# Kernel tuning notes

Measured on AMD Instinct MI355X. Metric: run time of the kernel, lower is better.

## Reference

```python
import jax, jax.numpy as jnp
import numpy as np

B, C, H, W_SP = 4, 64, 64, 64
CI = C // 2  # inter_channels = 32
DEPTH = 64
EPS = 1e-5


def conv2d(x, w, b, pad=0, dil=1):
    out = jax.lax.conv_general_dilated(
        x, w, window_strides=(1, 1),
        padding=[(pad, pad), (pad, pad)],
        rhs_dilation=(dil, dil),
        dimension_numbers=('NCHW', 'OIHW', 'NCHW'))
    return out + b[None, :, None, None]


def setup_inputs() -> dict:
    key = jax.random.key(0)
    ks = iter(jax.random.split(key, 32))
    nrm = lambda shp, s=0.01: jax.random.normal(next(ks), shp, jnp.float32) * s
    inp = {
        'x': jax.random.normal(next(ks), (B, C, H, W_SP), jnp.float32),
        # NonlocalBlock params (init: normal(0, 0.01), bias 0)
        'g_w': nrm((CI, C, 1, 1)), 'g_b': jnp.zeros((CI,), jnp.float32),
        'theta_w': nrm((CI, C, 1, 1)), 'theta_b': jnp.zeros((CI,), jnp.float32),
        'phi_w': nrm((CI, C, 1, 1)), 'phi_b': jnp.zeros((CI,), jnp.float32),
        'Wz_w': nrm((C, CI, 1, 1)), 'Wz_b': jnp.zeros((C,), jnp.float32),
        'bn_g': jax.random.normal(next(ks), (C,), jnp.float32),  # normal_(W[1].weight, 0) -> std 1
        'bn_b': jnp.zeros((C,), jnp.float32),
        # ASPP params (torch default kaiming init approximated by small normals)
        'a_mean_w': nrm((DEPTH, C, 1, 1), 0.05), 'a_mean_b': jnp.zeros((DEPTH,), jnp.float32),
        'a1_w': nrm((DEPTH, C, 1, 1), 0.05), 'a1_b': jnp.zeros((DEPTH,), jnp.float32),
        'a3_w': nrm((DEPTH, C, 3, 3), 0.02), 'a3_b': jnp.zeros((DEPTH,), jnp.float32),
        'a5_w': nrm((DEPTH, C, 3, 3), 0.02), 'a5_b': jnp.zeros((DEPTH,), jnp.float32),
        'a7_w': nrm((DEPTH, C, 3, 3), 0.02), 'a7_b': jnp.zeros((DEPTH,), jnp.float32),
        'out_w': nrm((DEPTH, DEPTH * 5, 1, 1), 0.02), 'out_b': jnp.zeros((DEPTH,), jnp.float32),
    }
    return inp


def _forward(x, g_w, g_b, theta_w, theta_b, phi_w, phi_b, Wz_w, Wz_b, bn_g, bn_b,
             a_mean_w, a_mean_b, a1_w, a1_b, a3_w, a3_b, a5_w, a5_b, a7_w, a7_b,
             out_w, out_b):
    b, c, h, w = x.shape
    n = h * w
    # ---- NonlocalBlock: global self-attention ----
    g_x = conv2d(x, g_w, g_b).reshape(b, CI, n).transpose(0, 2, 1)       # [B,N,Ci]
    theta_x = conv2d(x, theta_w, theta_b).reshape(b, CI, n).transpose(0, 2, 1)  # [B,N,Ci]
    phi_x = conv2d(x, phi_w, phi_b).reshape(b, CI, n)                    # [B,Ci,N]
    f = jnp.einsum('bqc,bck->bqk', theta_x, phi_x)                       # [B,N,N]
    f_div_C = jax.nn.softmax(f, axis=2)
    y = jnp.einsum('bqk,bkc->bqc', f_div_C, g_x)                         # [B,N,Ci]
    y = y.transpose(0, 2, 1).reshape(b, CI, h, w)
    wy = conv2d(y, Wz_w, Wz_b)
    # BatchNorm (eval: running_mean=0, running_var=1)
    wy = wy * (bn_g / jnp.sqrt(1.0 + EPS))[None, :, None, None] + bn_b[None, :, None, None]
    z = wy + x
    # ---- ASPP ----
    img = jnp.mean(z, axis=(2, 3), keepdims=True)                        # [B,C,1,1]
    img = conv2d(img, a_mean_w, a_mean_b)                                # [B,D,1,1]
    img = jnp.broadcast_to(img, (b, DEPTH, h, w))  # bilinear upsample of 1x1 is constant
    b1 = conv2d(z, a1_w, a1_b)
    b3 = conv2d(z, a3_w, a3_b, pad=3, dil=3)
    b5 = conv2d(z, a5_w, a5_b, pad=5, dil=5)
    b7 = conv2d(z, a7_w, a7_b, pad=7, dil=7)
    cat = jnp.concatenate([img, b1, b3, b5, b7], axis=1)                 # [B,5D,H,W]
    return conv2d(cat, out_w, out_b)                                     # [B,D,H,W]


def reference(x, g_w, g_b, theta_w, theta_b, phi_w, phi_b, Wz_w, Wz_b, bn_g, bn_b,
              a_mean_w, a_mean_b, a1_w, a1_b, a3_w, a3_b, a5_w, a5_b, a7_w, a7_b,
              out_w, out_b):
    return _forward(x, g_w, g_b, theta_w, theta_b, phi_w, phi_b, Wz_w, Wz_b, bn_g, bn_b,
                    a_mean_w, a_mean_b, a1_w, a1_b, a3_w, a3_b, a5_w, a5_b, a7_w, a7_b,
                    out_w, out_b)
```

## Files before the change

### kernel.cpp

```cpp
#include <hip/hip_runtime.h>


typedef __attribute__((ext_vector_type(8))) short bf16x8;
typedef __attribute__((ext_vector_type(4))) short s16x4;
typedef __attribute__((ext_vector_type(4))) float f32x4;

#define MFMA(a, b, c) __builtin_amdgcn_mfma_f32_16x16x32_bf16((a), (b), (c), 0, 0, 0)

#if __has_builtin(__builtin_amdgcn_exp2f)
#define EXP2(x) __builtin_amdgcn_exp2f(x)
#else
#define EXP2(x) exp2f(x)
#endif

__device__ static inline short f2bf(float f) {
  union { float f; unsigned u; } v; v.f = f;
  unsigned r = v.u + 0x7fffu + ((v.u >> 16) & 1u);
  return (short)(r >> 16);
}
__device__ static inline float bf2f(unsigned short h) {
  union { unsigned u; float f; } v; v.u = ((unsigned)h) << 16;
  return v.f;
}
__device__ static inline s16x4 pk4(f32x4 v) {
  s16x4 r; r.x = f2bf(v.x); r.y = f2bf(v.y); r.z = f2bf(v.z); r.w = f2bf(v.w);
  return r;
}
__device__ static inline unsigned pk2(float f0, float f1) {
  union { float f; unsigned u; } a, b; a.f = f0; b.f = f1;
  return __builtin_amdgcn_perm(b.u, a.u, 0x07060302u);
}
__device__ static inline float unlo(unsigned d) {
  union { unsigned u; float f; } v; v.u = d << 16; return v.f;
}
__device__ static inline float unhi(unsigned d) {
  union { unsigned u; float f; } v; v.u = d & 0xffff0000u; return v.f;
}
__device__ static inline f32x4 exp24(f32x4 v) {
  f32x4 r; r.x = EXP2(v.x); r.y = EXP2(v.y); r.z = EXP2(v.z); r.w = EXP2(v.w);
  return r;
}

#define QF_PER_B 131072
#define ZPB      389376
#define LOG2E    1.4426950408889634f

__global__ __launch_bounds__(256) void k_zero(unsigned* zp, float* zmean) {
  int blk = blockIdx.x, t = threadIdx.x;
  if (blk == 996) { if (t < 256) zmean[t] = 0.f; return; }
  int b = blk / 249, loc = blk - b * 249;
  int i = loc * 256 + t;
  if (i >= 63616) return;
  int px = i >> 5, dw = i & 31;
  int row, col;
  if (px < 1092) {
    int r = px / 78; col = px - r * 78;
    row = (r < 7) ? r : r + 64;
  } else {
    int j = px - 1092;
    int r = j / 14; int c = j - r * 14;
    row = r + 7; col = (c < 7) ? c : c + 57;
  }
  zp[b * (ZPB / 2) + (row * 78 + col) * 32 + dw] = 0u;
}

__global__ __launch_bounds__(256) void k_prep(
    const float* __restrict__ out_w, const float* __restrict__ a1_w,
    const float* __restrict__ a3_w, const float* __restrict__ a5_w,
    const float* __restrict__ a7_w, const float* __restrict__ Wz_w,
    const float* __restrict__ bn_g, const float* __restrict__ Wz_b,
    const float* __restrict__ bn_b,
    unsigned short* __restrict__ Wfrag, unsigned short* __restrict__ WzF,
    float* __restrict__ bias2) {
  int blk = blockIdx.x, t = threadIdx.x;
  if (blk < 28) {
    __shared__ float wsm[4096];
    __shared__ float osm[64 * 65];
    int tap = blk;
    const float* w; int goff, kyx = 0, ksq = 9;
    if (tap == 0)      { w = a1_w; goff = 64;  ksq = 1; }
    else if (tap < 10) { w = a3_w; goff = 128; kyx = tap - 1; }
    else if (tap < 19) { w = a5_w; goff = 192; kyx = tap - 10; }
    else               { w = a7_w; goff = 256; kyx = tap - 19; }
    for (int i = t; i < 4096; i += 256) {
      wsm[i] = w[i * ksq + kyx];
      int d = i >> 6, m = i & 63;
      osm[d * 65 + m] = out_w[d * 320 + goff + m];
    }
    __syncthreads();
    int dt = t >> 6, lane = t & 63, quad = lane >> 4, l15 = lane & 15;
    int d = dt * 16 + l15;
    float acc[16];
    #pragma unroll
    for (int k = 0; k < 16; ++k) acc[k] = 0.f;
    const float* orow = osm + d * 65;
    int c0 = quad * 8;
    for (int m = 0; m < 64; ++m) {
      float o = orow[m];
      const float* wr = wsm + m * 64 + c0;
      #pragma unroll
      for (int cc = 0; cc < 2; ++cc)
        #pragma unroll
        for (int j = 0; j < 8; ++j)
          acc[cc * 8 + j] += o * wr[cc * 32 + j];
    }
    #pragma unroll
    for (int cc = 0; cc < 2; ++cc) {
      bf16x8 v;
      #pragma unroll
      for (int j = 0; j < 8; ++j) v[j] = f2bf(acc[cc * 8 + j]);
      *(bf16x8*)(Wfrag + (((tap * 4 + dt) * 2 + cc) * 64 + lane) * 8) = v;
    }
  } else if (blk == 28) {
    int ct = t >> 6, lane = t & 63, quad = lane >> 4, l15 = lane & 15;
    int c = ct * 16 + l15;
    float s = bn_g[c] * rsqrtf(1.f + 1e-5f);
    bf16x8 v;
    #pragma unroll
    for (int j = 0; j < 8; ++j) v[j] = f2bf(s * Wz_w[c * 32 + quad * 8 + j]);
    *(bf16x8*)(WzF + (ct * 64 + lane) * 8) = v;
  } else if (t < 64) {
    float s = bn_g[t] * rsqrtf(1.f + 1e-5f);
    bias2[t] = s * Wz_b[t] + bn_b[t];
  }
}

__global__ __launch_bounds__(256) void k_qkv(
    const float* __restrict__ x,
    const float* __restrict__ tw, const float* __restrict__ tb,
    const float* __restrict__ pw, const float* __restrict__ pb,
    const float* __restrict__ gw, const float* __restrict__ gb,
    unsigned short* __restrict__ thetaB, unsigned short* __restrict__ phiB,
    unsigned short* __restrict__ gB) {
  __shared__ float wl[2048];
  __shared__ float bl[32];
  int blk = blockIdx.x;
  int b = blk & 3, pt = (blk >> 2) & 15, proj = blk >> 6;
  const float* w    = proj == 0 ? tw : (proj == 1 ? pw : gw);
  const float* bias = proj == 0 ? tb : (proj == 1 ? pb : gb);
  int tid = threadIdx.x;
  for (int i = tid; i < 2048; i += 256) wl[i] = w[i];
  if (tid < 32) bl[tid] = bias[tid];
  __syncthreads();
  int pix = pt*256 + tid;
  const float* xp = x + b*64*4096 + pix;
  float acc[32];
  #pragma unroll
  for (int ci = 0; ci < 32; ++ci) acc[ci] = bl[ci];
  for (int c = 0; c < 64; ++c) {
    float xv = xp[c*4096];
    #pragma unroll
    for (int ci = 0; ci < 32; ++ci) acc[ci] += wl[ci*64 + c] * xv;
  }
  if (proj == 0) {
    #pragma unroll
    for (int ci = 0; ci < 32; ++ci) acc[ci] *= LOG2E;
  }
  if (proj < 2) {
    unsigned short* base = (proj == 0 ? thetaB : phiB) + b*QF_PER_B
                           + (pix >> 4)*512 + (pix & 15)*8;
    #pragma unroll
    for (int q = 0; q < 4; ++q) {
      bf16x8 v;
      #pragma unroll
      for (int j = 0; j < 8; ++j) v[j] = f2bf(acc[q*8 + j]);
      *(bf16x8*)(base + q*128) = v;
    }
  } else {
    unsigned short* base = gB + b*QF_PER_B + (pix >> 5)*1024
                           + ((pix & 31) >> 3)*128 + (pix & 7);
    #pragma unroll
    for (int ci = 0; ci < 32; ++ci)
      base[(ci >> 4)*512 + (ci & 15)*8] = (unsigned short)f2bf(acc[ci]);
  }
}

__global__ __launch_bounds__(64) void k_attn(
    const unsigned short* __restrict__ thetaB, const unsigned short* __restrict__ phiB,
    const unsigned short* __restrict__ gB, unsigned* __restrict__ part) {
  __shared__ __align__(16) unsigned short plds[1152];
  int blk = blockIdx.x;
  int b = blk >> 9, qblk = (blk >> 2) & 127, kh = blk & 3;
  int lane = threadIdx.x, quad = lane >> 4, l15 = lane & 15;
  const bf16x8* thB = (const bf16x8*)(thetaB + b*QF_PER_B);
  const bf16x8* phF = (const bf16x8*)(phiB + b*QF_PER_B);
  const bf16x8* gF  = (const bf16x8*)(gB + b*QF_PER_B);
  bf16x8 th0 = thB[(qblk*2 + 0)*64 + lane];
  bf16x8 th1 = thB[(qblk*2 + 1)*64 + lane];
  bf16x8 ones;
  #pragma unroll
  for (int j = 0; j < 8; ++j) ones[j] = (short)0x3F80;
  const f32x4 z4 = {0.f, 0.f, 0.f, 0.f};
  f32x4 acc00 = z4, acc01 = z4, acc10 = z4, acc11 = z4;
  f32x4 accL0 = z4, accL1 = z4;
  unsigned short* r0p = plds + l15*36 + quad*4;
  unsigned short* r1p = plds + 576 + l15*36 + quad*4;
  const unsigned short* q0p = plds + l15*36 + quad*8;
  const unsigned short* q1p = plds + 576 + l15*36 + quad*8;
  int kt0 = kh*32;
  for (int kt = kt0; kt < kt0 + 32; ++kt) {
    int tbase = kt*128 + lane;
    bf16x8 pf0 = phF[tbase];
    bf16x8 pf1 = phF[tbase + 64];
    bf16x8 gf0 = gF[tbase];
    bf16x8 gf1 = gF[tbase + 64];
    f32x4 s00 = MFMA(pf0, th0, z4);
    f32x4 s10 = MFMA(pf1, th0, z4);
    f32x4 s01 = MFMA(pf0, th1, z4);
    f32x4 s11 = MFMA(pf1, th1, z4);
    f32x4 p00 = exp24(s00), p10 = exp24(s10), p01 = exp24(s01), p11 = exp24(s11);
    uint2 w0; w0.x = pk2(p00.x, p00.y); w0.y = pk2(p00.z, p00.w);
    uint2 w1; w1.x = pk2(p10.x, p10.y); w1.y = pk2(p10.z, p10.w);
    uint2 w2; w2.x = pk2(p01.x, p01.y); w2.y = pk2(p01.z, p01.w);
    uint2 w3; w3.x = pk2(p11.x, p11.y); w3.y = pk2(p11.z, p11.w);
    *(uint2*)(r0p)      = w0;
    *(uint2*)(r0p + 16) = w1;
    *(uint2*)(r1p)      = w2;
    *(uint2*)(r1p + 16) = w3;
    uint2 a0 = *(const uint2*)(q0p);
    uint2 a1 = *(const uint2*)(q0p + 4);
    uint2 b0 = *(const uint2*)(q1p);
    uint2 b1 = *(const uint2*)(q1p + 4);
    union { unsigned u[4]; bf16x8 v; } pb0c, pb1c;
    pb0c.u[0] = a0.x; pb0c.u[1] = a0.y; pb0c.u[2] = a1.x; pb0c.u[3] = a1.y;
    pb1c.u[0] = b0.x; pb1c.u[1] = b0.y; pb1c.u[2] = b1.x; pb1c.u[3] = b1.y;
    acc00 = MFMA(gf0, pb0c.v, acc00);
    acc01 = MFMA(gf1, pb0c.v, acc01);
    acc10 = MFMA(gf0, pb1c.v, acc10);
    acc11 = MFMA(gf1, pb1c.v, acc11);
    accL0 = MFMA(ones, pb0c.v, accL0);
    accL1 = MFMA(ones, pb1c.v, accL1);
  }
  unsigned* pp = part + blk*640;
  uint4 y0, y1;
  y0.x = pk2(acc00.x, acc00.y); y0.y = pk2(acc00.z, acc00.w);
  y0.z = pk2(acc01.x, acc01.y); y0.w = pk2(acc01.z, acc01.w);
  y1.x = pk2(acc10.x, acc10.y); y1.y = pk2(acc10.z, acc10.w);
  y1.z = pk2(acc11.x, acc11.y); y1.w = pk2(acc11.z, acc11.w);
  *(uint4*)(pp + lane*8)     = y0;
  *(uint4*)(pp + lane*8 + 4) = y1;
  float* lp = (float*)(pp + 512);
  lp[lane*2]     = accL0.x;
  lp[lane*2 + 1] = accL1.x;
}

__global__ __launch_bounds__(64) void k_merge(
    const unsigned* __restrict__ part, const unsigned short* __restrict__ WzF,
    const float* __restrict__ bias2, const float* __restrict__ x,
    unsigned short* __restrict__ z_pad) {
  __shared__ __align__(16) unsigned short ylds[1280];
  int blk = blockIdx.x;
  int b = blk >> 7, qblk = blk & 127;
  int lane = threadIdx.x, quad = lane >> 4, l15 = lane & 15;
  const f32x4 z4 = {0.f, 0.f, 0.f, 0.f};
  f32x4 a00 = z4, a01 = z4, a10 = z4, a11 = z4;
  float l0 = 0.f, l1 = 0.f;
  #pragma unroll
  for (int kh = 0; kh < 4; ++kh) {
    const unsigned* pp = part + (blk*4 + kh)*640;
    uint4 A = *(const uint4*)(pp + lane*8);
    uint4 B = *(const uint4*)(pp + lane*8 + 4);
    a00.x += unlo(A.x); a00.y += unhi(A.x); a00.z += unlo(A.y); a00.w += unhi(A.y);
    a01.x += unlo(A.z); a01.y += unhi(A.z); a01.z += unlo(A.w); a01.w += unhi(A.w);
    a10.x += unlo(B.x); a10.y += unhi(B.x); a10.z += unlo(B.y); a10.w += unhi(B.y);
    a11.x += unlo(B.z); a11.y += unhi(B.z); a11.z += unlo(B.w); a11.w += unhi(B.w);
    const float* lp = (const float*)(pp + 512);
    l0 += lp[lane*2]; l1 += lp[lane*2 + 1];
  }
  float r0 = 1.f / l0, r1 = 1.f / l1;
  a00 *= r0; a01 *= r0; a10 *= r1; a11 *= r1;
  *(s16x4*)(ylds + l15*40 + quad*4)             = pk4(a00);
  *(s16x4*)(ylds + l15*40 + 16 + quad*4)        = pk4(a01);
  *(s16x4*)(ylds + (16 + l15)*40 + quad*4)      = pk4(a10);
  *(s16x4*)(ylds + (16 + l15)*40 + 16 + quad*4) = pk4(a11);
  bf16x8 y0 = *(const bf16x8*)(ylds + l15*40 + quad*8);
  bf16x8 y1 = *(const bf16x8*)(ylds + (16 + l15)*40 + quad*8);
  const bf16x8* wzf = (const bf16x8*)WzF;
  int q0 = qblk * 32;
  #pragma unroll
  for (int ct = 0; ct < 4; ++ct) {
    bf16x8 wf = wzf[ct*64 + lane];
    f32x4 zq0 = MFMA(wf, y0, z4);
    f32x4 zq1 = MFMA(wf, y1, z4);
    int c0 = ct*16 + quad*4;
    f32x4 b2 = *(const f32x4*)(bias2 + c0);
    #pragma unroll
    for (int qt = 0; qt < 2; ++qt) {
      f32x4 zz = qt ? zq1 : zq0;
      int q = q0 + qt*16 + l15;
      int h = q >> 6, w = q & 63;
      const float* xp = x + (b*64 + c0)*4096 + q;
      s16x4 pkv;
      pkv.x = f2bf(zz.x + b2.x + xp[0]);
      pkv.y = f2bf(zz.y + b2.y + xp[4096]);
      pkv.z = f2bf(zz.z + b2.z + xp[8192]);
      pkv.w = f2bf(zz.w + b2.w + xp[12288]);
      *(s16x4*)(z_pad + b*ZPB + ((h + 7)*78 + (w + 7))*64 + c0) = pkv;
    }
  }
}

__global__ __launch_bounds__(256) void k_zmean(const unsigned short* __restrict__ z_pad,
                                               float* __restrict__ zmean) {
  __shared__ float red[256];
  int blk = blockIdx.x;
  int b = blk >> 6, ch = blk & 63;
  int t = threadIdx.x, c = t & 63, pg = t >> 6;
  const unsigned short* zp = z_pad + b*ZPB;
  float s = 0.f;
  for (int k = 0; k < 16; ++k) {
    int pix = ch*64 + pg*16 + k;
    int row = (pix >> 6) + 7, col = (pix & 63) + 7;
    s += bf2f(zp[(row*78 + col)*64 + c]);
  }
  red[t] = s;
  __syncthreads();
  if (t < 64)
    atomicAdd(zmean + b*64 + c, red[t] + red[64 + t] + red[128 + t] + red[192 + t]);
}

__global__ __launch_bounds__(64) void k_cb(
    const float* __restrict__ zmean, const float* __restrict__ am_w,
    const float* __restrict__ am_b, const float* __restrict__ out_w,
    const float* __restrict__ out_b, const float* __restrict__ a1_b,
    const float* __restrict__ a3_b, const float* __restrict__ a5_b,
    const float* __restrict__ a7_b, float* __restrict__ c_b) {
  __shared__ float img[64];
  int b = blockIdx.x, d = threadIdx.x;
  float s = am_b[d];
  for (int c = 0; c < 64; ++c)
    s += am_w[d*64 + c] * (zmean[b*64 + c] * (1.f / 4096.f));
  img[d] = s;
  __syncthreads();
  const float* ow = out_w + d*320;
  float r = out_b[d];
  for (int dd = 0; dd < 64; ++dd) r += ow[dd] * img[dd];
  for (int m = 0; m < 64; ++m)
    r += ow[64 + m]*a1_b[m] + ow[128 + m]*a3_b[m] + ow[192 + m]*a5_b[m] + ow[256 + m]*a7_b[m];
  c_b[b*64 + d] = r;
}

__global__ __launch_bounds__(64) void k_conv(
    const unsigned short* __restrict__ z_pad, const unsigned short* __restrict__ Wfrag,
    const float* __restrict__ c_b, float* __restrict__ out) {
  static constexpr int DYt[28] = {0, -3,-3,-3,0,0,0,3,3,3,
                                     -5,-5,-5,0,0,0,5,5,5,
                                     -7,-7,-7,0,0,0,7,7,7};
  static constexpr int DXt[28] = {0, -3,0,3,-3,0,3,-3,0,3,
                                     -5,0,5,-5,0,5,-5,0,5,
                                     -7,0,7,-7,0,7,-7,0,7};
  int blk = blockIdx.x;
  int b = blk >> 8, h = (blk >> 2) & 63, dt2 = (blk >> 1) & 1, wt2 = blk & 1;
  int lane = threadIdx.x, quad = lane >> 4, l15 = lane & 15;
  const unsigned short* zb = z_pad + b*ZPB + ((h + 7)*78 + 7)*64 + quad*8;
  const bf16x8* wfp = (const bf16x8*)Wfrag + lane;
  int d0 = dt2*2 + 0, d1 = dt2*2 + 1;
  f32x4 cb0 = *(const f32x4*)(c_b + b*64 + d0*16 + quad*4);
  f32x4 cb1 = *(const f32x4*)(c_b + b*64 + d1*16 + quad*4);
  f32x4 acc00 = cb0, acc01 = cb0, acc10 = cb1, acc11 = cb1;
  int col0 = ((wt2*2 + 0)*16 + l15)*64;
  int col1 = ((wt2*2 + 1)*16 + l15)*64;
  #pragma unroll
  for (int tap = 0; tap < 28; ++tap) {
    int toff = (DYt[tap]*78 + DXt[tap])*64;
    const unsigned short* zrow = zb + toff;
    #pragma unroll
    for (int cc = 0; cc < 2; ++cc) {
      bf16x8 zf0 = *(const bf16x8*)(zrow + col0 + cc*32);
      bf16x8 zf1 = *(const bf16x8*)(zrow + col1 + cc*32);
      bf16x8 wf0 = wfp[((tap*4 + d0)*2 + cc)*64];
      bf16x8 wf1 = wfp[((tap*4 + d1)*2 + cc)*64];
      acc00 = MFMA(wf0, zf0, acc00);
      acc01 = MFMA(wf0, zf1, acc01);
      acc10 = MFMA(wf1, zf0, acc10);
      acc11 = MFMA(wf1, zf1, acc11);
    }
  }
  float* ob = out + b*262144 + h*64;
  int w0 = (wt2*2 + 0)*16 + l15, w1 = (wt2*2 + 1)*16 + l15;
  int dd0 = d0*16 + quad*4, dd1 = d1*16 + quad*4;
  ob[(dd0 + 0)*4096 + w0] = acc00.x;
  ob[(dd0 + 1)*4096 + w0] = acc00.y;
  ob[(dd0 + 2)*4096 + w0] = acc00.z;
  ob[(dd0 + 3)*4096 + w0] = acc00.w;
  ob[(dd0 + 0)*4096 + w1] = acc01.x;
  ob[(dd0 + 1)*4096 + w1] = acc01.y;
  ob[(dd0 + 2)*4096 + w1] = acc01.z;
  ob[(dd0 + 3)*4096 + w1] = acc01.w;
  ob[(dd1 + 0)*4096 + w0] = acc10.x;
  ob[(dd1 + 1)*4096 + w0] = acc10.y;
  ob[(dd1 + 2)*4096 + w0] = acc10.z;
  ob[(dd1 + 3)*4096 + w0] = acc10.w;
  ob[(dd1 + 0)*4096 + w1] = acc11.x;
  ob[(dd1 + 1)*4096 + w1] = acc11.y;
  ob[(dd1 + 2)*4096 + w1] = acc11.z;
  ob[(dd1 + 3)*4096 + w1] = acc11.w;
}

extern "C" void kernel_launch(void* const* d_in, const int* in_sizes, int n_in,
                              void* d_out, int out_size, void* d_ws, size_t ws_size,
                              hipStream_t stream) {
  const float* x    = (const float*)d_in[0];
  const float* g_w  = (const float*)d_in[1];
  const float* g_b  = (const float*)d_in[2];
  const float* th_w = (const float*)d_in[3];
  const float* th_b = (const float*)d_in[4];
  const float* ph_w = (const float*)d_in[5];
  const float* ph_b = (const float*)d_in[6];
  const float* Wz_w = (const float*)d_in[7];
  const float* Wz_b = (const float*)d_in[8];
  const float* bn_g = (const float*)d_in[9];
  const float* bn_b = (const float*)d_in[10];
  const float* am_w = (const float*)d_in[11];
  const float* am_b = (const float*)d_in[12];
  const float* a1_w = (const float*)d_in[13];
  const float* a1_b = (const float*)d_in[14];
  const float* a3_w = (const float*)d_in[15];
  const float* a3_b = (const float*)d_in[16];
  const float* a5_w = (const float*)d_in[17];
  const float* a5_b = (const float*)d_in[18];
  const float* a7_w = (const float*)d_in[19];
  const float* a7_b = (const float*)d_in[20];
  const float* out_w = (const float*)d_in[21];
  const float* out_b = (const float*)d_in[22];
  float* out = (float*)d_out;
  char* ws = (char*)d_ws;
  unsigned short* thetaB = (unsigned short*)(ws + 0);
  unsigned short* phiB   = (unsigned short*)(ws + 1048576);
  unsigned short* gB     = (unsigned short*)(ws + 2097152);
  unsigned short* z_pad  = (unsigned short*)(ws + 3145728);
  unsigned short* Wfrag  = (unsigned short*)(ws + 6260736);
  unsigned short* WzF    = (unsigned short*)(ws + 6490112);
  float* zmean           = (float*)(ws + 6494208);
  float* c_b             = (float*)(ws + 6495232);
  float* bias2           = (float*)(ws + 6496256);
  unsigned* part         = (unsigned*)(ws + 6496512);

  k_zero<<<dim3(997), dim3(256), 0, stream>>>((unsigned*)z_pad, zmean);
  k_prep<<<dim3(30), dim3(256), 0, stream>>>(out_w, a1_w, a3_w, a5_w, a7_w,
                                             Wz_w, bn_g, Wz_b, bn_b, Wfrag, WzF, bias2);
  k_qkv<<<dim3(192), dim3(256), 0, stream>>>(x, th_w, th_b, ph_w, ph_b, g_w, g_b,
                                             thetaB, phiB, gB);
  k_attn<<<dim3(2048), dim3(64), 0, stream>>>(thetaB, phiB, gB, part);
  k_merge<<<dim3(512), dim3(64), 0, stream>>>(part, WzF, bias2, x, z_pad);
  k_zmean<<<dim3(256), dim3(256), 0, stream>>>(z_pad, zmean);
  k_cb<<<dim3(4), dim3(64), 0, stream>>>(zmean, am_w, am_b, out_w, out_b,
                                         a1_b, a3_b, a5_b, a7_b, c_b);
  k_conv<<<dim3(1024), dim3(64), 0, stream>>>(z_pad, Wfrag, c_b, out);
}
```

Baseline: 187.3 us.

## Fuse setup kernels and merge attention split-K reduction in shared memory

Combines the zero, weight-prep and QKV projection kernels into one launch that branches on block index. The attention kernel now uses 512-thread blocks where 8 waves split the key range and reduce their partial results through LDS. The softmax merge, Wz projection, residual add and z-mean atomics all happen in the same kernel, so the global partial buffer and the separate merge, zmean and cb kernels are gone. The image-pool bias is recomputed in each conv block with shuffles. This cuts the launch count from eight to three and removes partial-result global traffic, at the cost of redundant per-block bias math, fewer and larger attention blocks, and more atomics.

Result: faster. 182.2 us (-2.7%).

```diff
diff --git a/kernel.cpp b/kernel.cpp
--- a/kernel.cpp
+++ b/kernel.cpp
@@ -30,12 +30,6 @@
   union { float f; unsigned u; } a, b; a.f = f0; b.f = f1;
   return __builtin_amdgcn_perm(b.u, a.u, 0x07060302u);
 }
-__device__ static inline float unlo(unsigned d) {
-  union { unsigned u; float f; } v; v.u = d << 16; return v.f;
-}
-__device__ static inline float unhi(unsigned d) {
-  union { unsigned u; float f; } v; v.u = d & 0xffff0000u; return v.f;
-}
 __device__ static inline f32x4 exp24(f32x4 v) {
   f32x4 r; r.x = EXP2(v.x); r.y = EXP2(v.y); r.z = EXP2(v.z); r.w = EXP2(v.w);
   return r;
@@ -45,143 +39,165 @@
 #define ZPB      389376
 #define LOG2E    1.4426950408889634f
 
-__global__ __launch_bounds__(256) void k_zero(unsigned* zp, float* zmean) {
-  int blk = blockIdx.x, t = threadIdx.x;
-  if (blk == 996) { if (t < 256) zmean[t] = 0.f; return; }
-  int b = blk / 249, loc = blk - b * 249;
-  int i = loc * 256 + t;
-  if (i >= 63616) return;
-  int px = i >> 5, dw = i & 31;
-  int row, col;
-  if (px < 1092) {
-    int r = px / 78; col = px - r * 78;
-    row = (r < 7) ? r : r + 64;
-  } else {
-    int j = px - 1092;
-    int r = j / 14; int c = j - r * 14;
-    row = r + 7; col = (c < 7) ? c : c + 57;
-  }
-  zp[b * (ZPB / 2) + (row * 78 + col) * 32 + dw] = 0u;
-}
-
-__global__ __launch_bounds__(256) void k_prep(
-    const float* __restrict__ out_w, const float* __restrict__ a1_w,
-    const float* __restrict__ a3_w, const float* __restrict__ a5_w,
-    const float* __restrict__ a7_w, const float* __restrict__ Wz_w,
-    const float* __restrict__ bn_g, const float* __restrict__ Wz_b,
-    const float* __restrict__ bn_b,
-    unsigned short* __restrict__ Wfrag, unsigned short* __restrict__ WzF,
-    float* __restrict__ bias2) {
-  int blk = blockIdx.x, t = threadIdx.x;
-  if (blk < 28) {
-    __shared__ float wsm[4096];
-    __shared__ float osm[64 * 65];
-    int tap = blk;
-    const float* w; int goff, kyx = 0, ksq = 9;
-    if (tap == 0)      { w = a1_w; goff = 64;  ksq = 1; }
-    else if (tap < 10) { w = a3_w; goff = 128; kyx = tap - 1; }
-    else if (tap < 19) { w = a5_w; goff = 192; kyx = tap - 10; }
-    else               { w = a7_w; goff = 256; kyx = tap - 19; }
-    for (int i = t; i < 4096; i += 256) {
-      wsm[i] = w[i * ksq + kyx];
-      int d = i >> 6, m = i & 63;
-      osm[d * 65 + m] = out_w[d * 320 + goff + m];
-    }
-    __syncthreads();
-    int dt = t >> 6, lane = t & 63, quad = lane >> 4, l15 = lane & 15;
-    int d = dt * 16 + l15;
-    float acc[16];
-    #pragma unroll
-    for (int k = 0; k < 16; ++k) acc[k] = 0.f;
-    const float* orow = osm + d * 65;
-    int c0 = quad * 8;
-    for (int m = 0; m < 64; ++m) {
-      float o = orow[m];
-      const float* wr = wsm + m * 64 + c0;
-      #pragma unroll
-      for (int cc = 0; cc < 2; ++cc)
-        #pragma unroll
-        for (int j = 0; j < 8; ++j)
-          acc[cc * 8 + j] += o * wr[cc * 32 + j];
-    }
-    #pragma unroll
-    for (int cc = 0; cc < 2; ++cc) {
-      bf16x8 v;
-      #pragma unroll
-      for (int j = 0; j < 8; ++j) v[j] = f2bf(acc[cc * 8 + j]);
-      *(bf16x8*)(Wfrag + (((tap * 4 + dt) * 2 + cc) * 64 + lane) * 8) = v;
-    }
-  } else if (blk == 28) {
-    int ct = t >> 6, lane = t & 63, quad = lane >> 4, l15 = lane & 15;
-    int c = ct * 16 + l15;
-    float s = bn_g[c] * rsqrtf(1.f + 1e-5f);
-    bf16x8 v;
-    #pragma unroll
-    for (int j = 0; j < 8; ++j) v[j] = f2bf(s * Wz_w[c * 32 + quad * 8 + j]);
-    *(bf16x8*)(WzF + (ct * 64 + lane) * 8) = v;
-  } else if (t < 64) {
-    float s = bn_g[t] * rsqrtf(1.f + 1e-5f);
-    bias2[t] = s * Wz_b[t] + bn_b[t];
-  }
-}
-
-__global__ __launch_bounds__(256) void k_qkv(
+__global__ __launch_bounds__(256) void k_setup(
     const float* __restrict__ x,
     const float* __restrict__ tw, const float* __restrict__ tb,
     const float* __restrict__ pw, const float* __restrict__ pb,
     const float* __restrict__ gw, const float* __restrict__ gb,
+    const float* __restrict__ out_w, const float* __restrict__ out_b,
+    const float* __restrict__ a1_w, const float* __restrict__ a3_w,
+    const float* __restrict__ a5_w, const float* __restrict__ a7_w,
+    const float* __restrict__ a1_b, const float* __restrict__ a3_b,
+    const float* __restrict__ a5_b, const float* __restrict__ a7_b,
+    const float* __restrict__ Wz_w, const float* __restrict__ Wz_b,
+    const float* __restrict__ bn_g, const float* __restrict__ bn_b,
+    const float* __restrict__ am_w,
+    unsigned* __restrict__ zp, float* __restrict__ zmean,
+    unsigned short* __restrict__ Wfrag, unsigned short* __restrict__ WzF,
+    float* __restrict__ bias2,
     unsigned short* __restrict__ thetaB, unsigned short* __restrict__ phiB,
-    unsigned short* __restrict__ gB) {
-  __shared__ float wl[2048];
-  __shared__ float bl[32];
+    unsigned short* __restrict__ gB,
+    float* __restrict__ am_wT, float* __restrict__ owT0,
+    float* __restrict__ cbias) {
+  __shared__ union {
+    struct { float wsm[4096]; float osm[64 * 65]; } prep;
+    struct { float wl[2048]; float bl[32]; } qkv;
+  } sm;
+  int blk = blockIdx.x, t = threadIdx.x;
+  if (blk < 997) {
+    if (blk == 996) { if (t < 256) zmean[t] = 0.f; return; }
+    int b = blk / 249, loc = blk - b * 249;
+    int i = loc * 256 + t;
+    if (i >= 63616) return;
+    int px = i >> 5, dw = i & 31;
+    int row, col;
+    if (px < 1092) {
+      int r = px / 78; col = px - r * 78;
+      row = (r < 7) ? r : r + 64;
+    } else {
+      int j = px - 1092;
+      int r = j / 14; int c = j - r * 14;
+      row = r + 7; col = (c < 7) ? c : c + 57;
+    }
+    zp[b * (ZPB / 2) + (row * 78 + col) * 32 + dw] = 0u;
+  } else if (blk < 1027) {
+    int pblk = blk - 997;
+    if (pblk < 28) {
+      int tap = pblk;
+      const float* w; int goff, kyx = 0, ksq = 9;
+      if (tap == 0)      { w = a1_w; goff = 64;  ksq = 1; }
+      else if (tap < 10) { w = a3_w; goff = 128; kyx = tap - 1; }
+      else if (tap < 19) { w = a5_w; goff = 192; kyx = tap - 10; }
+      else               { w = a7_w; goff = 256; kyx = tap - 19; }
+      for (int i = t; i < 4096; i += 256) {
+        sm.prep.wsm[i] = w[i * ksq + kyx];
+        int d = i >> 6, m = i & 63;
+        sm.prep.osm[d * 65 + m] = out_w[d * 320 + goff + m];
+      }
+      __syncthreads();
+      int dt = t >> 6, lane = t & 63, quad = lane >> 4, l15 = lane & 15;
+      int d = dt * 16 + l15;
+      float acc[16];
+      #pragma unroll
+      for (int k = 0; k < 16; ++k) acc[k] = 0.f;
+      const float* orow = sm.prep.osm + d * 65;
+      int c0 = quad * 8;
+      for (int m = 0; m < 64; ++m) {
+        float o = orow[m];
+        const float* wr = sm.prep.wsm + m * 64 + c0;
+        #pragma unroll
+        for (int cc = 0; cc < 2; ++cc)
+          #pragma unroll
+          for (int j = 0; j < 8; ++j)
+            acc[cc * 8 + j] += o * wr[cc * 32 + j];
+      }
+      #pragma unroll
+      for (int cc = 0; cc < 2; ++cc) {
+        bf16x8 v;
+        #pragma unroll
+        for (int j = 0; j < 8; ++j) v[j] = f2bf(acc[cc * 8 + j]);
+        *(bf16x8*)(Wfrag + (((tap * 4 + dt) * 2 + cc) * 64 + lane) * 8) = v;
+      }
+    } else if (pblk == 28) {
+      int ct = t >> 6, lane = t & 63, quad = lane >> 4, l15 = lane & 15;
+      int c = ct * 16 + l15;
+      float s = bn_g[c] * rsqrtf(1.f + 1e-5f);
+      bf16x8 v;
+      #pragma unroll
+      for (int j = 0; j < 8; ++j) v[j] = f2bf(s * Wz_w[c * 32 + quad * 8 + j]);
+      *(bf16x8*)(WzF + (ct * 64 + lane) * 8) = v;
+    } else if (t < 64) {
+      float s = bn_g[t] * rsqrtf(1.f + 1e-5f);
+      bias2[t] = s * Wz_b[t] + bn_b[t];
+    }
+  } else if (blk < 1219) {
+    int qb = blk - 1027;
+    int b = qb & 3, pt = (qb >> 2) & 15, proj = qb >> 6;
+    const float* w    = proj == 0 ? tw : (proj == 1 ? pw : gw);
+    const float* bias = proj == 0 ? tb : (proj == 1 ? pb : gb);
+    for (int i = t; i < 2048; i += 256) sm.qkv.wl[i] = w[i];
+    if (t < 32) sm.qkv.bl[t] = bias[t];
+    __syncthreads();
+    int pix = pt*256 + t;
+    const float* xp = x + b*64*4096 + pix;
+    float acc[32];
+    #pragma unroll
+    for (int ci = 0; ci < 32; ++ci) acc[ci] = sm.qkv.bl[ci];
+    for (int c = 0; c < 64; ++c) {
+      float xv = xp[c*4096];
+      #pragma unroll
+      for (int ci = 0; ci < 32; ++ci) acc[ci] += sm.qkv.wl[ci*64 + c] * xv;
+    }
+    if (proj == 0) {
+      #pragma unroll
+      for (int ci = 0; ci < 32; ++ci) acc[ci] *= LOG2E;
+    }
+    if (proj < 2) {
+      unsigned short* base = (proj == 0 ? thetaB : phiB) + b*QF_PER_B
+                             + (pix >> 4)*512 + (pix & 15)*8;
+      #pragma unroll
+      for (int q = 0; q < 4; ++q) {
+        bf16x8 v;
+        #pragma unroll
+        for (int j = 0; j < 8; ++j) v[j] = f2bf(acc[q*8 + j]);
+        *(bf16x8*)(base + q*128) = v;
+      }
+    } else {
+      unsigned short* base = gB + b*QF_PER_B + (pix >> 5)*1024
+                             + ((pix & 31) >> 3)*128 + (pix & 7);
+      #pragma unroll
+      for (int ci = 0; ci < 32; ++ci)
+        base[(ci >> 4)*512 + (ci & 15)*8] = (unsigned short)f2bf(acc[ci]);
+    }
+  } else {
+    for (int i = t; i < 4096; i += 256) {
+      int d = i >> 6, c = i & 63;
+      am_wT[c * 64 + d] = am_w[i];
+      owT0[c * 64 + d] = out_w[d * 320 + c];
+    }
+    if (t < 64) {
+      float r = out_b[t];
+      const float* ow = out_w + t * 320;
+      for (int m = 0; m < 64; ++m)
+        r += ow[64 + m] * a1_b[m] + ow[128 + m] * a3_b[m]
+           + ow[192 + m] * a5_b[m] + ow[256 + m] * a7_b[m];
+      cbias[t] = r;
+    }
+  }
+}
+
+__global__ __launch_bounds__(512) void k_attn(
+    const unsigned short* __restrict__ thetaB, const unsigned short* __restrict__ phiB,
+    const unsigned short* __restrict__ gB, const unsigned short* __restrict__ WzF,
+    const float* __restrict__ bias2, const float* __restrict__ x,
+    unsigned short* __restrict__ z_pad, float* __restrict__ zmean) {
+  __shared__ float ypart[8][64][20];
+  __shared__ __align__(16) unsigned short plds[8][1152];
+  __shared__ __align__(16) unsigned short ytr[4][1280];
   int blk = blockIdx.x;
-  int b = blk & 3, pt = (blk >> 2) & 15, proj = blk >> 6;
-  const float* w    = proj == 0 ? tw : (proj == 1 ? pw : gw);
-  const float* bias = proj == 0 ? tb : (proj == 1 ? pb : gb);
+  int b = blk >> 7, qblk = blk & 127;
   int tid = threadIdx.x;
-  for (int i = tid; i < 2048; i += 256) wl[i] = w[i];
-  if (tid < 32) bl[tid] = bias[tid];
-  __syncthreads();
-  int pix = pt*256 + tid;
-  const float* xp = x + b*64*4096 + pix;
-  float acc[32];
-  #pragma unroll
-  for (int ci = 0; ci < 32; ++ci) acc[ci] = bl[ci];
-  for (int c = 0; c < 64; ++c) {
-    float xv = xp[c*4096];
-    #pragma unroll
-    for (int ci = 0; ci < 32; ++ci) acc[ci] += wl[ci*64 + c] * xv;
-  }
-  if (proj == 0) {
-    #pragma unroll
-    for (int ci = 0; ci < 32; ++ci) acc[ci] *= LOG2E;
-  }
-  if (proj < 2) {
-    unsigned short* base = (proj == 0 ? thetaB : phiB) + b*QF_PER_B
-                           + (pix >> 4)*512 + (pix & 15)*8;
-    #pragma unroll
-    for (int q = 0; q < 4; ++q) {
-      bf16x8 v;
-      #pragma unroll
-      for (int j = 0; j < 8; ++j) v[j] = f2bf(acc[q*8 + j]);
-      *(bf16x8*)(base + q*128) = v;
-    }
-  } else {
-    unsigned short* base = gB + b*QF_PER_B + (pix >> 5)*1024
-                           + ((pix & 31) >> 3)*128 + (pix & 7);
-    #pragma unroll
-    for (int ci = 0; ci < 32; ++ci)
-      base[(ci >> 4)*512 + (ci & 15)*8] = (unsigned short)f2bf(acc[ci]);
-  }
-}
-
-__global__ __launch_bounds__(64) void k_attn(
-    const unsigned short* __restrict__ thetaB, const unsigned short* __restrict__ phiB,
-    const unsigned short* __restrict__ gB, unsigned* __restrict__ part) {
-  __shared__ __align__(16) unsigned short plds[1152];
-  int blk = blockIdx.x;
-  int b = blk >> 9, qblk = (blk >> 2) & 127, kh = blk & 3;
-  int lane = threadIdx.x, quad = lane >> 4, l15 = lane & 15;
+  int kh = tid >> 6, lane = tid & 63, quad = lane >> 4, l15 = lane & 15;
   const bf16x8* thB = (const bf16x8*)(thetaB + b*QF_PER_B);
   const bf16x8* phF = (const bf16x8*)(phiB + b*QF_PER_B);
   const bf16x8* gF  = (const bf16x8*)(gB + b*QF_PER_B);
@@ -193,12 +209,13 @@
   const f32x4 z4 = {0.f, 0.f, 0.f, 0.f};
   f32x4 acc00 = z4, acc01 = z4, acc10 = z4, acc11 = z4;
   f32x4 accL0 = z4, accL1 = z4;
-  unsigned short* r0p = plds + l15*36 + quad*4;
-  unsigned short* r1p = plds + 576 + l15*36 + quad*4;
-  const unsigned short* q0p = plds + l15*36 + quad*8;
-  const unsigned short* q1p = plds + 576 + l15*36 + quad*8;
-  int kt0 = kh*32;
-  for (int kt = kt0; kt < kt0 + 32; ++kt) {
+  unsigned short* pl = &plds[kh][0];
+  unsigned short* r0p = pl + l15*36 + quad*4;
+  unsigned short* r1p = pl + 576 + l15*36 + quad*4;
+  const unsigned short* q0p = pl + l15*36 + quad*8;
+  const unsigned short* q1p = pl + 576 + l15*36 + quad*8;
+  int kt0 = kh*16;
+  for (int kt = kt0; kt < kt0 + 16; ++kt) {
     int tbase = kt*128 + lane;
     bf16x8 pf0 = phF[tbase];
     bf16x8 pf1 = phF[tbase + 64];
@@ -231,118 +248,78 @@
     accL0 = MFMA(ones, pb0c.v, accL0);
     accL1 = MFMA(ones, pb1c.v, accL1);
   }
-  unsigned* pp = part + blk*640;
-  uint4 y0, y1;
-  y0.x = pk2(acc00.x, acc00.y); y0.y = pk2(acc00.z, acc00.w);
-  y0.z = pk2(acc01.x, acc01.y); y0.w = pk2(acc01.z, acc01.w);
-  y1.x = pk2(acc10.x, acc10.y); y1.y = pk2(acc10.z, acc10.w);
-  y1.z = pk2(acc11.x, acc11.y); y1.w = pk2(acc11.z, acc11.w);
-  *(uint4*)(pp + lane*8)     = y0;
-  *(uint4*)(pp + lane*8 + 4) = y1;
-  float* lp = (float*)(pp + 512);
-  lp[lane*2]     = accL0.x;
-  lp[lane*2 + 1] = accL1.x;
-}
-
-__global__ __launch_bounds__(64) void k_merge(
-    const unsigned* __restrict__ part, const unsigned short* __restrict__ WzF,
-    const float* __restrict__ bias2, const float* __restrict__ x,
-    unsigned short* __restrict__ z_pad) {
-  __shared__ __align__(16) unsigned short ylds[1280];
-  int blk = blockIdx.x;
-  int b = blk >> 7, qblk = blk & 127;
-  int lane = threadIdx.x, quad = lane >> 4, l15 = lane & 15;
-  const f32x4 z4 = {0.f, 0.f, 0.f, 0.f};
+  float* yp = &ypart[kh][lane][0];
+  *(f32x4*)(yp + 0)  = acc00;
+  *(f32x4*)(yp + 4)  = acc01;
+  *(f32x4*)(yp + 8)  = acc10;
+  *(f32x4*)(yp + 12) = acc11;
+  yp[16] = accL0.x; yp[17] = accL1.x;
+  __syncthreads();
+  if (kh >= 4) return;
+  int ct = kh;
   f32x4 a00 = z4, a01 = z4, a10 = z4, a11 = z4;
   float l0 = 0.f, l1 = 0.f;
   #pragma unroll
-  for (int kh = 0; kh < 4; ++kh) {
-    const unsigned* pp = part + (blk*4 + kh)*640;
-    uint4 A = *(const uint4*)(pp + lane*8);
-    uint4 B = *(const uint4*)(pp + lane*8 + 4);
-    a00.x += unlo(A.x); a00.y += unhi(A.x); a00.z += unlo(A.y); a00.w += unhi(A.y);
-    a01.x += unlo(A.z); a01.y += unhi(A.z); a01.z += unlo(A.w); a01.w += unhi(A.w);
-    a10.x += unlo(B.x); a10.y += unhi(B.x); a10.z += unlo(B.y); a10.w += unhi(B.y);
-    a11.x += unlo(B.z); a11.y += unhi(B.z); a11.z += unlo(B.w); a11.w += unhi(B.w);
-    const float* lp = (const float*)(pp + 512);
-    l0 += lp[lane*2]; l1 += lp[lane*2 + 1];
+  for (int k = 0; k < 8; ++k) {
+    const float* q = &ypart[k][lane][0];
+    a00 += *(const f32x4*)(q + 0);
+    a01 += *(const f32x4*)(q + 4);
+    a10 += *(const f32x4*)(q + 8);
+    a11 += *(const f32x4*)(q + 12);
+    l0 += q[16]; l1 += q[17];
   }
   float r0 = 1.f / l0, r1 = 1.f / l1;
   a00 *= r0; a01 *= r0; a10 *= r1; a11 *= r1;
-  *(s16x4*)(ylds + l15*40 + quad*4)             = pk4(a00);
-  *(s16x4*)(ylds + l15*40 + 16 + quad*4)        = pk4(a01);
-  *(s16x4*)(ylds + (16 + l15)*40 + quad*4)      = pk4(a10);
-  *(s16x4*)(ylds + (16 + l15)*40 + 16 + quad*4) = pk4(a11);
-  bf16x8 y0 = *(const bf16x8*)(ylds + l15*40 + quad*8);
-  bf16x8 y1 = *(const bf16x8*)(ylds + (16 + l15)*40 + quad*8);
-  const bf16x8* wzf = (const bf16x8*)WzF;
-  int q0 = qblk * 32;
+  unsigned short* yl = &ytr[ct][0];
+  *(s16x4*)(yl + l15*40 + quad*4)             = pk4(a00);
+  *(s16x4*)(yl + l15*40 + 16 + quad*4)        = pk4(a01);
+  *(s16x4*)(yl + (16 + l15)*40 + quad*4)      = pk4(a10);
+  *(s16x4*)(yl + (16 + l15)*40 + 16 + quad*4) = pk4(a11);
+  bf16x8 y0 = *(const bf16x8*)(yl + l15*40 + quad*8);
+  bf16x8 y1 = *(const bf16x8*)(yl + (16 + l15)*40 + quad*8);
+  bf16x8 wf = ((const bf16x8*)WzF)[ct*64 + lane];
+  f32x4 zq0 = MFMA(wf, y0, z4);
+  f32x4 zq1 = MFMA(wf, y1, z4);
+  int c0 = ct*16 + quad*4;
+  f32x4 b2 = *(const f32x4*)(bias2 + c0);
+  int q0i = qblk * 32;
+  const float* xp0 = x + (b*64 + c0)*4096 + q0i + l15;
+  f32x4 s0, s1;
+  s0.x = zq0.x + b2.x + xp0[0];
+  s0.y = zq0.y + b2.y + xp0[4096];
+  s0.z = zq0.z + b2.z + xp0[8192];
+  s0.w = zq0.w + b2.w + xp0[12288];
+  s1.x = zq1.x + b2.x + xp0[16];
+  s1.y = zq1.y + b2.y + xp0[4096 + 16];
+  s1.z = zq1.z + b2.z + xp0[8192 + 16];
+  s1.w = zq1.w + b2.w + xp0[12288 + 16];
+  {
+    int q = q0i + l15, h = q >> 6, w = q & 63;
+    *(s16x4*)(z_pad + b*ZPB + ((h + 7)*78 + (w + 7))*64 + c0) = pk4(s0);
+    q = q0i + 16 + l15; h = q >> 6; w = q & 63;
+    *(s16x4*)(z_pad + b*ZPB + ((h + 7)*78 + (w + 7))*64 + c0) = pk4(s1);
+  }
+  f32x4 zs = s0 + s1;
   #pragma unroll
-  for (int ct = 0; ct < 4; ++ct) {
-    bf16x8 wf = wzf[ct*64 + lane];
-    f32x4 zq0 = MFMA(wf, y0, z4);
-    f32x4 zq1 = MFMA(wf, y1, z4);
-    int c0 = ct*16 + quad*4;
-    f32x4 b2 = *(const f32x4*)(bias2 + c0);
-    #pragma unroll
-    for (int qt = 0; qt < 2; ++qt) {
-      f32x4 zz = qt ? zq1 : zq0;
-      int q = q0 + qt*16 + l15;
-      int h = q >> 6, w = q & 63;
-      const float* xp = x + (b*64 + c0)*4096 + q;
-      s16x4 pkv;
-      pkv.x = f2bf(zz.x + b2.x + xp[0]);
-      pkv.y = f2bf(zz.y + b2.y + xp[4096]);
-      pkv.z = f2bf(zz.z + b2.z + xp[8192]);
-      pkv.w = f2bf(zz.w + b2.w + xp[12288]);
-      *(s16x4*)(z_pad + b*ZPB + ((h + 7)*78 + (w + 7))*64 + c0) = pkv;
-    }
-  }
-}
-
-__global__ __launch_bounds__(256) void k_zmean(const unsigned short* __restrict__ z_pad,
-                                               float* __restrict__ zmean) {
-  __shared__ float red[256];
-  int blk = blockIdx.x;
-  int b = blk >> 6, ch = blk & 63;
-  int t = threadIdx.x, c = t & 63, pg = t >> 6;
-  const unsigned short* zp = z_pad + b*ZPB;
-  float s = 0.f;
-  for (int k = 0; k < 16; ++k) {
-    int pix = ch*64 + pg*16 + k;
-    int row = (pix >> 6) + 7, col = (pix & 63) + 7;
-    s += bf2f(zp[(row*78 + col)*64 + c]);
-  }
-  red[t] = s;
-  __syncthreads();
-  if (t < 64)
-    atomicAdd(zmean + b*64 + c, red[t] + red[64 + t] + red[128 + t] + red[192 + t]);
-}
-
-__global__ __launch_bounds__(64) void k_cb(
-    const float* __restrict__ zmean, const float* __restrict__ am_w,
-    const float* __restrict__ am_b, const float* __restrict__ out_w,
-    const float* __restrict__ out_b, const float* __restrict__ a1_b,
-    const float* __restrict__ a3_b, const float* __restrict__ a5_b,
-    const float* __restrict__ a7_b, float* __restrict__ c_b) {
-  __shared__ float img[64];
-  int b = blockIdx.x, d = threadIdx.x;
-  float s = am_b[d];
-  for (int c = 0; c < 64; ++c)
-    s += am_w[d*64 + c] * (zmean[b*64 + c] * (1.f / 4096.f));
-  img[d] = s;
-  __syncthreads();
-  const float* ow = out_w + d*320;
-  float r = out_b[d];
-  for (int dd = 0; dd < 64; ++dd) r += ow[dd] * img[dd];
-  for (int m = 0; m < 64; ++m)
-    r += ow[64 + m]*a1_b[m] + ow[128 + m]*a3_b[m] + ow[192 + m]*a5_b[m] + ow[256 + m]*a7_b[m];
-  c_b[b*64 + d] = r;
+  for (int m = 1; m < 16; m <<= 1) {
+    zs.x += __shfl_xor(zs.x, m);
+    zs.y += __shfl_xor(zs.y, m);
+    zs.z += __shfl_xor(zs.z, m);
+    zs.w += __shfl_xor(zs.w, m);
+  }
+  if (l15 == 0) {
+    atomicAdd(zmean + b*64 + c0 + 0, zs.x);
+    atomicAdd(zmean + b*64 + c0 + 1, zs.y);
+    atomicAdd(zmean + b*64 + c0 + 2, zs.z);
+    atomicAdd(zmean + b*64 + c0 + 3, zs.w);
+  }
 }
 
 __global__ __launch_bounds__(64) void k_conv(
     const unsigned short* __restrict__ z_pad, const unsigned short* __restrict__ Wfrag,
-    const float* __restrict__ c_b, float* __restrict__ out) {
+    const float* __restrict__ zmean, const float* __restrict__ am_wT,
+    const float* __restrict__ am_b, const float* __restrict__ owT0,
+    const float* __restrict__ cbias, float* __restrict__ out) {
   static constexpr int DYt[28] = {0, -3,-3,-3,0,0,0,3,3,3,
                                      -5,-5,-5,0,0,0,5,5,5,
                                      -7,-7,-7,0,0,0,7,7,7};
@@ -352,12 +329,16 @@
   int blk = blockIdx.x;
   int b = blk >> 8, h = (blk >> 2) & 63, dt2 = (blk >> 1) & 1, wt2 = blk & 1;
   int lane = threadIdx.x, quad = lane >> 4, l15 = lane & 15;
+  float zml = zmean[b*64 + lane] * (1.f / 4096.f);
+  float img = am_b[lane];
+  for (int c = 0; c < 64; ++c) img += am_wT[c*64 + lane] * __shfl(zml, c);
+  float cbd = cbias[lane];
+  for (int dd = 0; dd < 64; ++dd) cbd += owT0[dd*64 + lane] * __shfl(img, dd);
   const unsigned short* zb = z_pad + b*ZPB + ((h + 7)*78 + 7)*64 + quad*8;
   const bf16x8* wfp = (const bf16x8*)Wfrag + lane;
   int d0 = dt2*2 + 0, d1 = dt2*2 + 1;
-  f32x4 cb0 = *(const f32x4*)(c_b + b*64 + d0*16 + quad*4);
-  f32x4 cb1 = *(const f32x4*)(c_b + b*64 + d1*16 + quad*4);
-  f32x4 acc00 = cb0, acc01 = cb0, acc10 = cb1, acc11 = cb1;
+  const f32x4 z4 = {0.f, 0.f, 0.f, 0.f};
+  f32x4 acc00 = z4, acc01 = z4, acc10 = z4, acc11 = z4;
   int col0 = ((wt2*2 + 0)*16 + l15)*64;
   int col1 = ((wt2*2 + 1)*16 + l15)*64;
   #pragma unroll
@@ -376,9 +357,15 @@
       acc11 = MFMA(wf1, zf1, acc11);
     }
   }
+  int dd0 = d0*16 + quad*4, dd1 = d1*16 + quad*4;
+  f32x4 cb0v, cb1v;
+  cb0v.x = __shfl(cbd, dd0 + 0); cb0v.y = __shfl(cbd, dd0 + 1);
+  cb0v.z = __shfl(cbd, dd0 + 2); cb0v.w = __shfl(cbd, dd0 + 3);
+  cb1v.x = __shfl(cbd, dd1 + 0); cb1v.y = __shfl(cbd, dd1 + 1);
+  cb1v.z = __shfl(cbd, dd1 + 2); cb1v.w = __shfl(cbd, dd1 + 3);
+  acc00 += cb0v; acc01 += cb0v; acc10 += cb1v; acc11 += cb1v;
   float* ob = out + b*262144 + h*64;
   int w0 = (wt2*2 + 0)*16 + l15, w1 = (wt2*2 + 1)*16 + l15;
-  int dd0 = d0*16 + quad*4, dd1 = d1*16 + quad*4;
   ob[(dd0 + 0)*4096 + w0] = acc00.x;
   ob[(dd0 + 1)*4096 + w0] = acc00.y;
   ob[(dd0 + 2)*4096 + w0] = acc00.z;
@@ -432,19 +419,19 @@
   unsigned short* Wfrag  = (unsigned short*)(ws + 6260736);
   unsigned short* WzF    = (unsigned short*)(ws + 6490112);
   float* zmean           = (float*)(ws + 6494208);
-  float* c_b             = (float*)(ws + 6495232);
-  float* bias2           = (float*)(ws + 6496256);
-  unsigned* part         = (unsigned*)(ws + 6496512);
-
-  k_zero<<<dim3(997), dim3(256), 0, stream>>>((unsigned*)z_pad, zmean);
-  k_prep<<<dim3(30), dim3(256), 0, stream>>>(out_w, a1_w, a3_w, a5_w, a7_w,
-                                             Wz_w, bn_g, Wz_b, bn_b, Wfrag, WzF, bias2);
-  k_qkv<<<dim3(192), dim3(256), 0, stream>>>(x, th_w, th_b, ph_w, ph_b, g_w, g_b,
-                                             thetaB, phiB, gB);
-  k_attn<<<dim3(2048), dim3(64), 0, stream>>>(thetaB, phiB, gB, part);
-  k_merge<<<dim3(512), dim3(64), 0, stream>>>(part, WzF, bias2, x, z_pad);
-  k_zmean<<<dim3(256), dim3(256), 0, stream>>>(z_pad, zmean);
-  k_cb<<<dim3(4), dim3(64), 0, stream>>>(zmean, am_w, am_b, out_w, out_b,
-                                         a1_b, a3_b, a5_b, a7_b, c_b);
-  k_conv<<<dim3(1024), dim3(64), 0, stream>>>(z_pad, Wfrag, c_b, out);
-}
+  float* bias2           = (float*)(ws + 6495232);
+  float* am_wT           = (float*)(ws + 6495488);
+  float* owT0            = (float*)(ws + 6511872);
+  float* cbias           = (float*)(ws + 6528256);
+
+  k_setup<<<dim3(1220), dim3(256), 0, stream>>>(
+      x, th_w, th_b, ph_w, ph_b, g_w, g_b, out_w, out_b,
+      a1_w, a3_w, a5_w, a7_w, a1_b, a3_b, a5_b, a7_b,
+      Wz_w, Wz_b, bn_g, bn_b, am_w,
+      (unsigned*)z_pad, zmean, Wfrag, WzF, bias2,
+      thetaB, phiB, gB, am_wT, owT0, cbias);
+  k_attn<<<dim3(512), dim3(512), 0, stream>>>(thetaB, phiB, gB, WzF, bias2, x,
+                                              z_pad, zmean);
+  k_conv<<<dim3(1024), dim3(64), 0, stream>>>(z_pad, Wfrag, zmean, am_wT, am_b,
+                                              owT0, cbias, out);
+}
```
